# Optimization experiments

Hardware: AMD Instinct MI355X
Metric: run time of the kernel (lower is better)

## Reference

```python
import jax, jax.numpy as jnp
import numpy as np

N = 50000
IN_DIM = 128
HEADS = 4
HEAD_DIM = IN_DIM // HEADS
TYPE_NUM = 3
E = 800000
NEG_SLOPE = 0.2


def setup_inputs() -> dict:
    key = jax.random.key(0)
    k1, k2, k3, k4, k5 = jax.random.split(key, 5)
    embedding = jax.random.normal(k1, (N, IN_DIM), dtype=jnp.float32)
    edges = jax.random.randint(k2, (TYPE_NUM, 2, E), 0, N, dtype=jnp.int32)
    W = jax.random.normal(k3, (TYPE_NUM, IN_DIM, HEADS, HEAD_DIM), dtype=jnp.float32) * 0.05
    a_src = jax.random.normal(k4, (TYPE_NUM, HEADS, HEAD_DIM), dtype=jnp.float32) * 0.05
    a_dst = jax.random.normal(k5, (TYPE_NUM, HEADS, HEAD_DIM), dtype=jnp.float32) * 0.05
    return {"embedding": embedding, "edges": edges, "W": W, "a_src": a_src, "a_dst": a_dst}


def _gat_layer(x, ei, W_t, asrc_t, adst_t):
    # x: [N, IN_DIM]; ei: [2, E]; W_t: [IN_DIM, H, D]
    h = jnp.einsum('nd,dhk->nhk', x, W_t)                  # [N, H, D]
    e_src = jnp.sum(h * asrc_t, axis=-1)                   # [N, H]
    e_dst = jnp.sum(h * adst_t, axis=-1)                   # [N, H]
    src, dst = ei[0], ei[1]
    e = jax.nn.leaky_relu(e_src[src] + e_dst[dst], NEG_SLOPE)  # [E, H]
    m = jax.ops.segment_max(e, dst, num_segments=N)        # [N, H]
    e = jnp.exp(e - m[dst])
    denom = jax.ops.segment_sum(e, dst, num_segments=N)    # [N, H]
    msg = h[src] * e[:, :, None]                           # [E, H, D]
    agg = jax.ops.segment_sum(msg, dst, num_segments=N)    # [N, H, D]
    out = agg / (denom[:, :, None] + 1e-9)
    return jax.nn.elu(out.reshape(N, HEADS * HEAD_DIM))


def reference(embedding, edges, W, a_src, a_dst):
    features_gat = [_gat_layer(embedding, edges[i], W[i], a_src[i], a_dst[i])
                    for i in range(TYPE_NUM)]
    # NOTE: the original module (faithfully) also uses the GAT layers for the
    # 'gcn' branch: features_gcn = [self.gat_layers[i](...) for ...]
    features_gcn = [_gat_layer(embedding, edges[i], W[i], a_src[i], a_dst[i])
                    for i in range(TYPE_NUM)]
    return (jnp.stack(features_gat), jnp.stack(features_gcn))
```

## Files before the change

### kernel.cpp

```cpp
#include <hip/hip_runtime.h>
#include <hip/hip_fp16.h>
#include <math.h>

#define NN 50000
#define IND 128
#define NH 4
#define NE 800000
#define NT 3
#define NSLOPE 0.2f

#define TILE 48
#define NBPT 1042
#define NBTOT (NT * NBPT)
#define BCAP 960
#define SRTCAP (BCAP + 3 * TILE)
#define DUMMY 0xFFFFu

#define SEB 8192
#define SCB ((NT * NE + SEB - 1) / SEB)
#define GXB ((NN + 127) / 128)

typedef _Float16 f16x8 __attribute__((ext_vector_type(8)));
typedef float    f32x4 __attribute__((ext_vector_type(4)));

__device__ __forceinline__ unsigned pk_add_f16(unsigned a, unsigned b) {
    __half2 x = *reinterpret_cast<__half2*>(&a);
    __half2 y = *reinterpret_cast<__half2*>(&b);
    __half2 r = __hadd2(x, y);
    return *reinterpret_cast<unsigned*>(&r);
}

__global__ __launch_bounds__(256) void prep_kernel(
    const float* __restrict__ W, __half* __restrict__ wt16g, int* __restrict__ gcursor)
{
    int idx = blockIdx.x * 256 + threadIdx.x;
    if (idx < NT * IND * IND) {
        int t = idx / (IND * IND), r = idx - t * (IND * IND);
        int k = r >> 7, c = r & 127;
        wt16g[((size_t)t * IND + c) * IND + k] = (__half)W[idx];
    }
    if (idx < NBTOT) gcursor[idx] = idx * BCAP;
}

__global__ __launch_bounds__(512) void scatter_gemm_kernel(
    const int* __restrict__ edges, int* __restrict__ gcursor, unsigned* __restrict__ bucketed,
    const float* __restrict__ x, const __half* __restrict__ wt16g,
    const float* __restrict__ asrc, const float* __restrict__ adst,
    __half* __restrict__ h16, float* __restrict__ es, float* __restrict__ ed)
{
    __shared__ __align__(16) char ldsbuf[34816];
    const int tid = threadIdx.x;

    if (blockIdx.x < SCB) {
        int* cnt = (int*)ldsbuf;
        int* bas = cnt + NBTOT;
        for (int i = tid; i < NBTOT; i += 512) cnt[i] = 0;
        __syncthreads();
        const long long gtot = (long long)NT * NE;
        const long long g0 = (long long)blockIdx.x * SEB;
        long long g1 = g0 + SEB; if (g1 > gtot) g1 = gtot;
        for (long long g = g0 + tid; g < g1; g += 512) {
            int t = (g >= 2LL * NE) ? 2 : (g >= NE ? 1 : 0);
            int e = (int)(g - (long long)t * NE);
            int d = edges[(size_t)t * 2 * NE + NE + e];
            atomicAdd(&cnt[t * NBPT + d / TILE], 1);
        }
        __syncthreads();
        for (int i = tid; i < NBTOT; i += 512) {
            int c = cnt[i];
            bas[i] = c ? atomicAdd(&gcursor[i], c) : 0;
            cnt[i] = 0;
        }
        __syncthreads();
        for (long long g = g0 + tid; g < g1; g += 512) {
            int t = (g >= 2LL * NE) ? 2 : (g >= NE ? 1 : 0);
            int e = (int)(g - (long long)t * NE);
            const int* eb = edges + (size_t)t * 2 * NE;
            int s = eb[e], d = eb[NE + e];
            int bkt = d / TILE;
            int bg = t * NBPT + bkt;
            int pos = bas[bg] + atomicAdd(&cnt[bg], 1);
            bucketed[pos] = (unsigned)s | ((unsigned)(d - bkt * TILE) << 16);
        }
        return;
    }

    const int bx = blockIdx.x - SCB;
    const int t  = bx / GXB;
    const int gx = bx - t * GXB;
    __half* tile = (__half*)ldsbuf;
    const int wid = tid >> 6, lane = tid & 63;
    __half* tl = tile + wid * (16 * 136);
    const int l15 = lane & 15, l4 = lane >> 4;
    const int r0 = gx * 128 + wid * 16;
    if (r0 >= NN) return;

    const __half* wt = wt16g + (size_t)t * IND * IND;
    const float* xrow = x + (size_t)(r0 + l15) * IND;

    f32x4 acc[8];
    #pragma unroll
    for (int i = 0; i < 8; i++) acc[i] = (f32x4){0.f, 0.f, 0.f, 0.f};

    #pragma unroll
    for (int ks = 0; ks < 4; ks++) {
        const int kb = ks * 32 + l4 * 8;
        float4 x0 = *reinterpret_cast<const float4*>(xrow + kb);
        float4 x1 = *reinterpret_cast<const float4*>(xrow + kb + 4);
        f16x8 af;
        af[0] = (_Float16)x0.x; af[1] = (_Float16)x0.y;
        af[2] = (_Float16)x0.z; af[3] = (_Float16)x0.w;
        af[4] = (_Float16)x1.x; af[5] = (_Float16)x1.y;
        af[6] = (_Float16)x1.z; af[7] = (_Float16)x1.w;
        #pragma unroll
        for (int ct = 0; ct < 8; ct++) {
            f16x8 bf = *reinterpret_cast<const f16x8*>(wt + (size_t)(ct * 16 + l15) * IND + kb);
            acc[ct] = __builtin_amdgcn_mfma_f32_16x16x32_f16(af, bf, acc[ct], 0, 0, 0);
        }
    }

    #pragma unroll
    for (int ct = 0; ct < 8; ct++)
        #pragma unroll
        for (int r = 0; r < 4; r++)
            tl[(l4 * 4 + r) * 136 + ct * 16 + l15] = (__half)acc[ct][r];
    __syncthreads();

    {
        #pragma unroll
        for (int i = 0; i < 4; i++) {
            int c = lane + 64 * i;
            int row = c >> 4, off = (c & 15) * 8;
            f16x8 v = *reinterpret_cast<const f16x8*>(tl + row * 136 + off);
            *reinterpret_cast<f16x8*>(h16 + ((size_t)t * NN + r0 + row) * IND + off) = v;
        }
        int row16 = lane >> 2, head = lane & 3;
        const __half* hr = tl + row16 * 136 + head * 32;
        const float* av = asrc + ((size_t)t * NH + head) * 32;
        const float* bv = adst + ((size_t)t * NH + head) * 32;
        float se = 0.f, de = 0.f;
        #pragma unroll
        for (int jj = 0; jj < 4; jj++) {
            f16x8 hv = *reinterpret_cast<const f16x8*>(hr + jj * 8);
            #pragma unroll
            for (int j = 0; j < 8; j++) {
                float hf = (float)hv[j];
                se = fmaf(hf, av[jj * 8 + j], se);
                de = fmaf(hf, bv[jj * 8 + j], de);
            }
        }
        int n = r0 + row16;
        es[((size_t)t * NN + n) * NH + head] = se;
        ed[((size_t)t * NN + n) * NH + head] = de;
    }
}

__global__ __launch_bounds__(512) void gat_bucket_kernel(
    const unsigned* __restrict__ bucketed, const int* __restrict__ gcursor,
    const float* __restrict__ es, const float* __restrict__ ed,
    const __half* __restrict__ h16, float* __restrict__ out)
{
    __shared__ unsigned pk[BCAP];
    __shared__ unsigned srt[SRTCAP];
    __shared__ int hist[64], scn[64], cur[64];
    const int bg = blockIdx.x;
    const int t = bg / NBPT;
    const int node0 = (bg - t * NBPT) * TILE;
    const int tid = threadIdx.x;
    const int base = bg * BCAP;
    const int cnt = gcursor[bg] - base;

    if (tid < 64) { hist[tid] = 0; cur[tid] = 0; }
    __syncthreads();
    for (int i = tid; i < cnt; i += 512) {
        unsigned v = __builtin_nontemporal_load(&bucketed[base + i]);
        pk[i] = v;
        atomicAdd(&hist[(v >> 16) & 63u], 1);
    }
    __syncthreads();
    if (tid < 64) {
        int v = hist[tid];
        int v4 = (v + 3) & ~3;
        int inc = v4;
        #pragma unroll
        for (int off = 1; off < 64; off <<= 1) {
            int n = __shfl_up(inc, off, 64);
            if (tid >= off) inc += n;
        }
        scn[tid] = inc - v4;
    }
    __syncthreads();
    for (int i = tid; i < cnt; i += 512) {
        unsigned v = pk[i];
        int dl = (int)((v >> 16) & 63u);
        int pos = scn[dl] + atomicAdd(&cur[dl], 1);
        srt[pos] = v & 0xFFFFu;
    }
    if (tid < 64) {
        int h = hist[tid], h4 = (h + 3) & ~3, b = scn[tid];
        for (int i = h; i < h4; i++) srt[b + i] = DUMMY;
    }
    __syncthreads();

    const int wid = tid >> 6, lane = tid & 63;
    const int el2 = lane >> 4;
    const int dl3 = lane & 15;
    const int hsel = dl3 >> 2;
    const float* es_t = es + (size_t)t * NN * NH;
    const __half* h16_t = h16 + (size_t)t * NN * IND;

    for (int j = 0; j < 6; j++) {
        const int dloc = wid * 6 + j;
        const int node = node0 + dloc;
        if (node >= NN) break;
        const int beg = scn[dloc];
        const int nE = (hist[dloc] + 3) & ~3;
        const float edv = ed[((size_t)t * NN + node) * NH + (lane & 3)];

        unsigned p0 = 0u, p1 = 0u, p2 = 0u, p3 = 0u;
        float dsum = 0.f;

        for (int b2 = 0; b2 < nE; b2 += 16) {
            int ne = nE - b2; if (ne > 16) ne = 16;
            const int ei = lane >> 2;
            int sv = 0; unsigned wpk = 0u;
            if (ei < ne) {
                unsigned svr = srt[beg + b2 + ei];
                if (svr != DUMMY) {
                    float s = es_t[(svr << 2) + (lane & 3)] + edv;
                    s = s > 0.f ? s : NSLOPE * s;
                    float wv = __expf(s);
                    dsum += wv;
                    __half2 w2 = __float2half2_rn(wv);
                    wpk = *reinterpret_cast<unsigned*>(&w2);
                    sv = (int)svr;
                }
            }
            for (int kk = 0; kk < ne; kk += 4) {
                int sl = (kk + el2) << 2;
                int      sb = __shfl(sv, sl, 64);
                unsigned wb = (unsigned)__shfl((int)wpk, sl | hsel, 64);
                uint4 hv = *reinterpret_cast<const uint4*>(h16_t + ((size_t)sb << 7) + (dl3 << 3));
                asm("v_pk_fma_f16 %0, %1, %2, %0" : "+v"(p0) : "v"(hv.x), "v"(wb));
                asm("v_pk_fma_f16 %0, %1, %2, %0" : "+v"(p1) : "v"(hv.y), "v"(wb));
                asm("v_pk_fma_f16 %0, %1, %2, %0" : "+v"(p2) : "v"(hv.z), "v"(wb));
                asm("v_pk_fma_f16 %0, %1, %2, %0" : "+v"(p3) : "v"(hv.w), "v"(wb));
            }
        }

        #pragma unroll
        for (int m = 4; m <= 32; m <<= 1) dsum += __shfl_xor(dsum, m, 64);
        #pragma unroll
        for (int m = 16; m <= 32; m <<= 1) {
            p0 = pk_add_f16(p0, (unsigned)__shfl_xor((int)p0, m, 64));
            p1 = pk_add_f16(p1, (unsigned)__shfl_xor((int)p1, m, 64));
            p2 = pk_add_f16(p2, (unsigned)__shfl_xor((int)p2, m, 64));
            p3 = pk_add_f16(p3, (unsigned)__shfl_xor((int)p3, m, 64));
        }
        float dn = __shfl(dsum, hsel, 64) + 1e-9f;

        if (el2 == 0) {
            float rn = 1.f / dn;
            float2 f0 = __half22float2(*reinterpret_cast<__half2*>(&p0));
            float2 f1 = __half22float2(*reinterpret_cast<__half2*>(&p1));
            float2 f2 = __half22float2(*reinterpret_cast<__half2*>(&p2));
            float2 f3 = __half22float2(*reinterpret_cast<__half2*>(&p3));
            float v0=f0.x*rn, v1=f0.y*rn, v2=f1.x*rn, v3=f1.y*rn;
            float v4=f2.x*rn, v5=f2.y*rn, v6=f3.x*rn, v7=f3.y*rn;
            f32x4 o0, o1;
            o0[0] = v0 > 0.f ? v0 : expm1f(v0);
            o0[1] = v1 > 0.f ? v1 : expm1f(v1);
            o0[2] = v2 > 0.f ? v2 : expm1f(v2);
            o0[3] = v3 > 0.f ? v3 : expm1f(v3);
            o1[0] = v4 > 0.f ? v4 : expm1f(v4);
            o1[1] = v5 > 0.f ? v5 : expm1f(v5);
            o1[2] = v6 > 0.f ? v6 : expm1f(v6);
            o1[3] = v7 > 0.f ? v7 : expm1f(v7);
            float* obase = out + (size_t)t * NN * IND + ((size_t)node << 7) + (dl3 << 3);
            float* obase2 = obase + (size_t)NT * NN * IND;
            __builtin_nontemporal_store(o0, reinterpret_cast<f32x4*>(obase));
            __builtin_nontemporal_store(o1, reinterpret_cast<f32x4*>(obase + 4));
            __builtin_nontemporal_store(o0, reinterpret_cast<f32x4*>(obase2));
            __builtin_nontemporal_store(o1, reinterpret_cast<f32x4*>(obase2 + 4));
        }
    }
}

extern "C" void kernel_launch(void* const* d_in, const int* in_sizes, int n_in,
                              void* d_out, int out_size, void* d_ws, size_t ws_size,
                              hipStream_t stream)
{
    const float* x     = (const float*)d_in[0];
    const int*   edges = (const int*)d_in[1];
    const float* W     = (const float*)d_in[2];
    const float* asrc  = (const float*)d_in[3];
    const float* adst  = (const float*)d_in[4];
    float* out = (float*)d_out;

    char* p = (char*)d_ws;
    __half*   h16      = (__half*)p;   p += (size_t)NT * NN * IND * 2;
    float*    es       = (float*)p;    p += (size_t)NT * NN * NH * 4;
    float*    ed       = (float*)p;    p += (size_t)NT * NN * NH * 4;
    int*      gcursor  = (int*)p;      p += (size_t)NBTOT * 4;
    __half*   wt16g    = (__half*)p;   p += (size_t)NT * IND * IND * 2;
    unsigned* bucketed = (unsigned*)p; p += ((size_t)NBTOT * BCAP + 1024) * 4;

    prep_kernel<<<(NT * IND * IND + 255) / 256, 256, 0, stream>>>(W, wt16g, gcursor);
    scatter_gemm_kernel<<<SCB + NT * GXB, 512, 0, stream>>>(
        edges, gcursor, bucketed, x, wt16g, asrc, adst, h16, es, ed);
    gat_bucket_kernel<<<NBTOT, 512, 0, stream>>>(bucketed, gcursor, es, ed, h16, out);
}
```

Before: 201.6 us.

## Pipeline per-type GEMM with previous type's GAT aggregation across launches

The projection GEMM is split per edge type and interleaved with the aggregation kernels. The first launch does the edge scatter plus GEMM for type 0, and each following launch aggregates type t while computing the GEMM for type t+1. The goal is to overlap the compute-heavy GEMM with the memory-bound gather and cut the serial GEMM phase. In exchange there are two extra kernel launches, and the aggregation for each type now runs in a smaller grid, which may leave the device underfilled.

```diff
diff --git a/kernel.cpp b/kernel.cpp
--- a/kernel.cpp
+++ b/kernel.cpp
@@ -42,52 +42,12 @@
     if (idx < NBTOT) gcursor[idx] = idx * BCAP;
 }
 
-__global__ __launch_bounds__(512) void scatter_gemm_kernel(
-    const int* __restrict__ edges, int* __restrict__ gcursor, unsigned* __restrict__ bucketed,
+__device__ __forceinline__ void gemm_body(
+    char* ldsbuf, int t, int gx, int tid,
     const float* __restrict__ x, const __half* __restrict__ wt16g,
     const float* __restrict__ asrc, const float* __restrict__ adst,
     __half* __restrict__ h16, float* __restrict__ es, float* __restrict__ ed)
 {
-    __shared__ __align__(16) char ldsbuf[34816];
-    const int tid = threadIdx.x;
-
-    if (blockIdx.x < SCB) {
-        int* cnt = (int*)ldsbuf;
-        int* bas = cnt + NBTOT;
-        for (int i = tid; i < NBTOT; i += 512) cnt[i] = 0;
-        __syncthreads();
-        const long long gtot = (long long)NT * NE;
-        const long long g0 = (long long)blockIdx.x * SEB;
-        long long g1 = g0 + SEB; if (g1 > gtot) g1 = gtot;
-        for (long long g = g0 + tid; g < g1; g += 512) {
-            int t = (g >= 2LL * NE) ? 2 : (g >= NE ? 1 : 0);
-            int e = (int)(g - (long long)t * NE);
-            int d = edges[(size_t)t * 2 * NE + NE + e];
-            atomicAdd(&cnt[t * NBPT + d / TILE], 1);
-        }
-        __syncthreads();
-        for (int i = tid; i < NBTOT; i += 512) {
-            int c = cnt[i];
-            bas[i] = c ? atomicAdd(&gcursor[i], c) : 0;
-            cnt[i] = 0;
-        }
-        __syncthreads();
-        for (long long g = g0 + tid; g < g1; g += 512) {
-            int t = (g >= 2LL * NE) ? 2 : (g >= NE ? 1 : 0);
-            int e = (int)(g - (long long)t * NE);
-            const int* eb = edges + (size_t)t * 2 * NE;
-            int s = eb[e], d = eb[NE + e];
-            int bkt = d / TILE;
-            int bg = t * NBPT + bkt;
-            int pos = bas[bg] + atomicAdd(&cnt[bg], 1);
-            bucketed[pos] = (unsigned)s | ((unsigned)(d - bkt * TILE) << 16);
-        }
-        return;
-    }
-
-    const int bx = blockIdx.x - SCB;
-    const int t  = bx / GXB;
-    const int gx = bx - t * GXB;
     __half* tile = (__half*)ldsbuf;
     const int wid = tid >> 6, lane = tid & 63;
     __half* tl = tile + wid * (16 * 136);
@@ -126,47 +86,46 @@
             tl[(l4 * 4 + r) * 136 + ct * 16 + l15] = (__half)acc[ct][r];
     __syncthreads();
 
-    {
-        #pragma unroll
-        for (int i = 0; i < 4; i++) {
-            int c = lane + 64 * i;
-            int row = c >> 4, off = (c & 15) * 8;
-            f16x8 v = *reinterpret_cast<const f16x8*>(tl + row * 136 + off);
-            *reinterpret_cast<f16x8*>(h16 + ((size_t)t * NN + r0 + row) * IND + off) = v;
-        }
-        int row16 = lane >> 2, head = lane & 3;
-        const __half* hr = tl + row16 * 136 + head * 32;
-        const float* av = asrc + ((size_t)t * NH + head) * 32;
-        const float* bv = adst + ((size_t)t * NH + head) * 32;
-        float se = 0.f, de = 0.f;
-        #pragma unroll
-        for (int jj = 0; jj < 4; jj++) {
-            f16x8 hv = *reinterpret_cast<const f16x8*>(hr + jj * 8);
-            #pragma unroll
-            for (int j = 0; j < 8; j++) {
-                float hf = (float)hv[j];
-                se = fmaf(hf, av[jj * 8 + j], se);
-                de = fmaf(hf, bv[jj * 8 + j], de);
-            }
-        }
-        int n = r0 + row16;
-        es[((size_t)t * NN + n) * NH + head] = se;
-        ed[((size_t)t * NN + n) * NH + head] = de;
-    }
-}
-
-__global__ __launch_bounds__(512) void gat_bucket_kernel(
+    #pragma unroll
+    for (int i = 0; i < 4; i++) {
+        int c = lane + 64 * i;
+        int row = c >> 4, off = (c & 15) * 8;
+        f16x8 v = *reinterpret_cast<const f16x8*>(tl + row * 136 + off);
+        *reinterpret_cast<f16x8*>(h16 + ((size_t)t * NN + r0 + row) * IND + off) = v;
+    }
+    int row16 = lane >> 2, head = lane & 3;
+    const __half* hr = tl + row16 * 136 + head * 32;
+    const float* av = asrc + ((size_t)t * NH + head) * 32;
+    const float* bv = adst + ((size_t)t * NH + head) * 32;
+    float se = 0.f, de = 0.f;
+    #pragma unroll
+    for (int jj = 0; jj < 4; jj++) {
+        f16x8 hv = *reinterpret_cast<const f16x8*>(hr + jj * 8);
+        #pragma unroll
+        for (int j = 0; j < 8; j++) {
+            float hf = (float)hv[j];
+            se = fmaf(hf, av[jj * 8 + j], se);
+            de = fmaf(hf, bv[jj * 8 + j], de);
+        }
+    }
+    int n = r0 + row16;
+    es[((size_t)t * NN + n) * NH + head] = se;
+    ed[((size_t)t * NN + n) * NH + head] = de;
+}
+
+__device__ __forceinline__ void gat_body(
+    char* ldsbuf, int t, int lb, int tid,
     const unsigned* __restrict__ bucketed, const int* __restrict__ gcursor,
     const float* __restrict__ es, const float* __restrict__ ed,
     const __half* __restrict__ h16, float* __restrict__ out)
 {
-    __shared__ unsigned pk[BCAP];
-    __shared__ unsigned srt[SRTCAP];
-    __shared__ int hist[64], scn[64], cur[64];
-    const int bg = blockIdx.x;
-    const int t = bg / NBPT;
-    const int node0 = (bg - t * NBPT) * TILE;
-    const int tid = threadIdx.x;
+    int* hist = (int*)ldsbuf;
+    int* scn  = hist + 64;
+    int* cur  = scn + 64;
+    unsigned* pk  = (unsigned*)(cur + 64);
+    unsigned* srt = pk + BCAP;
+    const int bg = t * NBPT + lb;
+    const int node0 = lb * TILE;
     const int base = bg * BCAP;
     const int cnt = gcursor[bg] - base;
 
@@ -286,6 +245,68 @@
     }
 }
 
+__global__ __launch_bounds__(512) void k_scatter_gemm(
+    const int* __restrict__ edges, int* __restrict__ gcursor, unsigned* __restrict__ bucketed,
+    const float* __restrict__ x, const __half* __restrict__ wt16g,
+    const float* __restrict__ asrc, const float* __restrict__ adst,
+    __half* __restrict__ h16, float* __restrict__ es, float* __restrict__ ed)
+{
+    __shared__ __align__(16) char ldsbuf[34816];
+    const int tid = threadIdx.x;
+
+    if (blockIdx.x < SCB) {
+        int* cnt = (int*)ldsbuf;
+        int* bas = cnt + NBTOT;
+        for (int i = tid; i < NBTOT; i += 512) cnt[i] = 0;
+        __syncthreads();
+        const long long gtot = (long long)NT * NE;
+        const long long g0 = (long long)blockIdx.x * SEB;
+        long long g1 = g0 + SEB; if (g1 > gtot) g1 = gtot;
+        for (long long g = g0 + tid; g < g1; g += 512) {
+            int t = (g >= 2LL * NE) ? 2 : (g >= NE ? 1 : 0);
+            int e = (int)(g - (long long)t * NE);
+            int d = edges[(size_t)t * 2 * NE + NE + e];
+            atomicAdd(&cnt[t * NBPT + d / TILE], 1);
+        }
+        __syncthreads();
+        for (int i = tid; i < NBTOT; i += 512) {
+            int c = cnt[i];
+            bas[i] = c ? atomicAdd(&gcursor[i], c) : 0;
+            cnt[i] = 0;
+        }
+        __syncthreads();
+        for (long long g = g0 + tid; g < g1; g += 512) {
+            int t = (g >= 2LL * NE) ? 2 : (g >= NE ? 1 : 0);
+            int e = (int)(g - (long long)t * NE);
+            const int* eb = edges + (size_t)t * 2 * NE;
+            int s = eb[e], d = eb[NE + e];
+            int bkt = d / TILE;
+            int bg = t * NBPT + bkt;
+            int pos = bas[bg] + atomicAdd(&cnt[bg], 1);
+            bucketed[pos] = (unsigned)s | ((unsigned)(d - bkt * TILE) << 16);
+        }
+        return;
+    }
+    gemm_body(ldsbuf, 0, blockIdx.x - SCB, tid, x, wt16g, asrc, adst, h16, es, ed);
+}
+
+__global__ __launch_bounds__(512) void k_gat_gemm(
+    int tg, int tm,
+    const unsigned* __restrict__ bucketed, const int* __restrict__ gcursor,
+    const float* __restrict__ x, const __half* __restrict__ wt16g,
+    const float* __restrict__ asrc, const float* __restrict__ adst,
+    __half* __restrict__ h16, float* __restrict__ es, float* __restrict__ ed,
+    float* __restrict__ out)
+{
+    __shared__ __align__(16) char ldsbuf[34816];
+    const int tid = threadIdx.x;
+    if ((int)blockIdx.x < NBPT) {
+        gat_body(ldsbuf, tg, blockIdx.x, tid, bucketed, gcursor, es, ed, h16, out);
+        return;
+    }
+    gemm_body(ldsbuf, tm, blockIdx.x - NBPT, tid, x, wt16g, asrc, adst, h16, es, ed);
+}
+
 extern "C" void kernel_launch(void* const* d_in, const int* in_sizes, int n_in,
                               void* d_out, int out_size, void* d_ws, size_t ws_size,
                               hipStream_t stream)
@@ -306,7 +327,12 @@
     unsigned* bucketed = (unsigned*)p; p += ((size_t)NBTOT * BCAP + 1024) * 4;
 
     prep_kernel<<<(NT * IND * IND + 255) / 256, 256, 0, stream>>>(W, wt16g, gcursor);
-    scatter_gemm_kernel<<<SCB + NT * GXB, 512, 0, stream>>>(
+    k_scatter_gemm<<<SCB + GXB, 512, 0, stream>>>(
         edges, gcursor, bucketed, x, wt16g, asrc, adst, h16, es, ed);
-    gat_bucket_kernel<<<NBTOT, 512, 0, stream>>>(bucketed, gcursor, es, ed, h16, out);
-}
+    k_gat_gemm<<<NBPT + GXB, 512, 0, stream>>>(
+        0, 1, bucketed, gcursor, x, wt16g, asrc, adst, h16, es, ed, out);
+    k_gat_gemm<<<NBPT + GXB, 512, 0, stream>>>(
+        1, 2, bucketed, gcursor, x, wt16g, asrc, adst, h16, es, ed, out);
+    k_gat_gemm<<<NBPT, 512, 0, stream>>>(
+        2, 0, bucketed, gcursor, x, wt16g, asrc, adst, h16, es, ed, out);
+}
```

Measured after the change: 239.6 us. 18.9% more time.

## Bucket edges into coarse 512-node chunks and filter per 64-node tile in gather

Applied to the files above, without the earlier changes.

Edge scattering now groups edges into 512-node coarse buckets instead of 48-node buckets, cutting the number of global cursor atomics and scattered writes. Each gather block of 64 nodes reads its entire coarse bucket and filters entries belonging to its slice using a shared counter, then sorts as before. This trades a cheaper scatter for eight-fold redundant reads of bucketed data in the gather and a contended shared atomic.

```diff
diff --git a/kernel.cpp b/kernel.cpp
--- a/kernel.cpp
+++ b/kernel.cpp
@@ -9,11 +9,14 @@
 #define NT 3
 #define NSLOPE 0.2f
 
-#define TILE 48
-#define NBPT 1042
+#define TILE 64
+#define NBPT 782
 #define NBTOT (NT * NBPT)
-#define BCAP 960
-#define SRTCAP (BCAP + 3 * TILE)
+#define NCPT 98
+#define NCB (NT * NCPT)
+#define CBCAP 8960
+#define FCAP 1312
+#define SRTCAP (FCAP + 3 * TILE)
 #define DUMMY 0xFFFFu
 
 #define SEB 8192
@@ -39,7 +42,7 @@
         int k = r >> 7, c = r & 127;
         wt16g[((size_t)t * IND + c) * IND + k] = (__half)W[idx];
     }
-    if (idx < NBTOT) gcursor[idx] = idx * BCAP;
+    if (idx < NCB) gcursor[idx] = idx * CBCAP;
 }
 
 __global__ __launch_bounds__(512) void scatter_gemm_kernel(
@@ -53,8 +56,8 @@
 
     if (blockIdx.x < SCB) {
         int* cnt = (int*)ldsbuf;
-        int* bas = cnt + NBTOT;
-        for (int i = tid; i < NBTOT; i += 512) cnt[i] = 0;
+        int* bas = cnt + NCB;
+        for (int i = tid; i < NCB; i += 512) cnt[i] = 0;
         __syncthreads();
         const long long gtot = (long long)NT * NE;
         const long long g0 = (long long)blockIdx.x * SEB;
@@ -63,10 +66,10 @@
             int t = (g >= 2LL * NE) ? 2 : (g >= NE ? 1 : 0);
             int e = (int)(g - (long long)t * NE);
             int d = edges[(size_t)t * 2 * NE + NE + e];
-            atomicAdd(&cnt[t * NBPT + d / TILE], 1);
+            atomicAdd(&cnt[t * NCPT + (d >> 9)], 1);
         }
         __syncthreads();
-        for (int i = tid; i < NBTOT; i += 512) {
+        for (int i = tid; i < NCB; i += 512) {
             int c = cnt[i];
             bas[i] = c ? atomicAdd(&gcursor[i], c) : 0;
             cnt[i] = 0;
@@ -77,10 +80,9 @@
             int e = (int)(g - (long long)t * NE);
             const int* eb = edges + (size_t)t * 2 * NE;
             int s = eb[e], d = eb[NE + e];
-            int bkt = d / TILE;
-            int bg = t * NBPT + bkt;
-            int pos = bas[bg] + atomicAdd(&cnt[bg], 1);
-            bucketed[pos] = (unsigned)s | ((unsigned)(d - bkt * TILE) << 16);
+            int cb = t * NCPT + (d >> 9);
+            int pos = bas[cb] + atomicAdd(&cnt[cb], 1);
+            bucketed[pos] = (unsigned)s | ((unsigned)(d & 511) << 16);
         }
         return;
     }
@@ -160,22 +162,31 @@
     const float* __restrict__ es, const float* __restrict__ ed,
     const __half* __restrict__ h16, float* __restrict__ out)
 {
-    __shared__ unsigned pk[BCAP];
+    __shared__ unsigned flist[FCAP];
     __shared__ unsigned srt[SRTCAP];
     __shared__ int hist[64], scn[64], cur[64];
+    __shared__ int nf;
     const int bg = blockIdx.x;
     const int t = bg / NBPT;
-    const int node0 = (bg - t * NBPT) * TILE;
+    const int lb = bg - t * NBPT;
+    const int node0 = lb * TILE;
     const int tid = threadIdx.x;
-    const int base = bg * BCAP;
-    const int cnt = gcursor[bg] - base;
+    const int cb = t * NCPT + (node0 >> 9);
+    const int slice = (node0 >> 6) & 7;
+    const int cbase = cb * CBCAP;
+    const int ccnt = gcursor[cb] - cbase;
 
     if (tid < 64) { hist[tid] = 0; cur[tid] = 0; }
-    __syncthreads();
-    for (int i = tid; i < cnt; i += 512) {
-        unsigned v = __builtin_nontemporal_load(&bucketed[base + i]);
-        pk[i] = v;
-        atomicAdd(&hist[(v >> 16) & 63u], 1);
+    if (tid == 0) nf = 0;
+    __syncthreads();
+    for (int i = tid; i < ccnt; i += 512) {
+        unsigned v = bucketed[cbase + i];
+        int dd = (int)((v >> 16) & 511u);
+        if ((dd >> 6) == slice) {
+            int pos = atomicAdd(&nf, 1);
+            flist[pos] = (v & 0xFFFFu) | ((unsigned)(dd & 63) << 16);
+            atomicAdd(&hist[dd & 63], 1);
+        }
     }
     __syncthreads();
     if (tid < 64) {
@@ -190,8 +201,9 @@
         scn[tid] = inc - v4;
     }
     __syncthreads();
-    for (int i = tid; i < cnt; i += 512) {
-        unsigned v = pk[i];
+    const int nfl = nf;
+    for (int i = tid; i < nfl; i += 512) {
+        unsigned v = flist[i];
         int dl = (int)((v >> 16) & 63u);
         int pos = scn[dl] + atomicAdd(&cur[dl], 1);
         srt[pos] = v & 0xFFFFu;
@@ -209,8 +221,8 @@
     const float* es_t = es + (size_t)t * NN * NH;
     const __half* h16_t = h16 + (size_t)t * NN * IND;
 
-    for (int j = 0; j < 6; j++) {
-        const int dloc = wid * 6 + j;
+    for (int j = 0; j < 8; j++) {
+        const int dloc = wid * 8 + j;
         const int node = node0 + dloc;
         if (node >= NN) break;
         const int beg = scn[dloc];
@@ -301,9 +313,9 @@
     __half*   h16      = (__half*)p;   p += (size_t)NT * NN * IND * 2;
     float*    es       = (float*)p;    p += (size_t)NT * NN * NH * 4;
     float*    ed       = (float*)p;    p += (size_t)NT * NN * NH * 4;
-    int*      gcursor  = (int*)p;      p += (size_t)NBTOT * 4;
+    int*      gcursor  = (int*)p;      p += (size_t)NCB * 4;
     __half*   wt16g    = (__half*)p;   p += (size_t)NT * IND * IND * 2;
-    unsigned* bucketed = (unsigned*)p; p += ((size_t)NBTOT * BCAP + 1024) * 4;
+    unsigned* bucketed = (unsigned*)p; p += ((size_t)NCB * CBCAP + 1024) * 4;
 
     prep_kernel<<<(NT * IND * IND + 255) / 256, 256, 0, stream>>>(W, wt16g, gcursor);
     scatter_gemm_kernel<<<SCB + NT * GXB, 512, 0, stream>>>(
```

New measurement: 229.3 us. +13.7%, slower.
